# Kernel optimization log

Measured on AMD Instinct MI355X. Metric: run time of the kernel, lower is better.

Reference implementation:

```python
import jax, jax.numpy as jnp
import numpy as np

B, L, D, H = 2, 2048, 1024, 16
HD = D // H  # head_dim = 64


def setup_inputs() -> dict:
    key = jax.random.key(0)
    k1, k2, k3, k4, k5 = jax.random.split(key, 5)
    s = 1.0 / np.sqrt(D)
    return {
        "x": jax.random.normal(k1, (B, L, D), dtype=jnp.float32),
        "quantum_scores": jax.random.normal(k2, (B, L, L), dtype=jnp.float32),
        "wq": jax.random.normal(k3, (D, D), dtype=jnp.float32) * s,
        "wk": jax.random.normal(k4, (D, D), dtype=jnp.float32) * s,
        "wv": jax.random.normal(k5, (D, D), dtype=jnp.float32) * s,
        "scale": jnp.ones((H, 1, 1), dtype=jnp.float32),
    }


def reference(x, quantum_scores, wq, wk, wv, scale):
    Bq, Lq, _ = x.shape
    # nn.Linear: y = x @ W^T ; then split heads -> (B, H, L, HD)
    def split_heads(t):
        return t.reshape(Bq, Lq, H, HD).transpose(0, 2, 1, 3)

    q = split_heads(x @ wq.T)
    k = split_heads(x @ wk.T)
    v = split_heads(x @ wv.T)

    logits = jnp.einsum("bhqd,bhkd->bhqk", q, k) / np.sqrt(HD).astype(np.float32)
    logits = logits + quantum_scores[:, None, :, :]          # quantum bias, broadcast over heads
    logits = logits * scale[None, :, :, :]                   # per-head learnable scale
    attn = jax.nn.softmax(logits, axis=-1)
    out = jnp.einsum("bhqk,bhkd->bhqd", attn, v)
    return out.transpose(0, 2, 1, 3).reshape(Bq, Lq, D)
```

## Files before the change

kernel.cpp:

```cpp
#include <hip/hip_runtime.h>

#define Bq 2
#define Lq 2048
#define Dq 1024
#define Hq 16
#define HDq 64

typedef _Float16 f16;
typedef _Float16 f16x8 __attribute__((ext_vector_type(8)));
typedef _Float16 f16x4 __attribute__((ext_vector_type(4)));
typedef __fp16 hf16x2 __attribute__((ext_vector_type(2)));
typedef float f32x4 __attribute__((ext_vector_type(4)));
typedef float f32x16 __attribute__((ext_vector_type(16)));

__device__ __forceinline__ void gload_lds16(const void* g, void* l) {
    __builtin_amdgcn_global_load_lds(
        (const __attribute__((address_space(1))) unsigned int*)g,
        (__attribute__((address_space(3))) unsigned int*)l, 16, 0, 0);
}

__device__ __forceinline__ void swap32(int& a, int& b) {
    asm volatile("v_permlane32_swap_b32 %0, %1" : "+v"(a), "+v"(b));
}

__device__ __forceinline__ int pk2(float a, float b) {
    hf16x2 v = __builtin_amdgcn_cvt_pkrtz(a, b);
    return __builtin_bit_cast(int, v);
}

__global__ __launch_bounds__(256) void convert_kernel(
    const float* __restrict__ x,
    const float* __restrict__ wq, const float* __restrict__ wk, const float* __restrict__ wv,
    f16* __restrict__ x_h, f16* __restrict__ wq_h, f16* __restrict__ wk_h, f16* __restrict__ wv_h)
{
    const int NX = Bq*Lq*Dq;
    const int NW = Dq*Dq;
    const int total4 = (NX + 3*NW) / 4;
    for (int i = blockIdx.x*blockDim.x + threadIdx.x; i < total4;
         i += gridDim.x*blockDim.x) {
        int e = i * 4;
        const float* src; f16* dst; int off;
        if (e < NX) { src = x; dst = x_h; off = e; }
        else {
            int t = e - NX; int w = t >> 20; off = t & (NW-1);
            src = (w==0) ? wq : (w==1) ? wk : wv;
            dst = (w==0) ? wq_h : (w==1) ? wk_h : wv_h;
        }
        float4 v = *reinterpret_cast<const float4*>(src + off);
        f16x4 hv; hv.x=(f16)v.x; hv.y=(f16)v.y; hv.z=(f16)v.z; hv.w=(f16)v.w;
        *reinterpret_cast<f16x4*>(dst + off) = hv;
    }
}

#define GBM 128
#define GBN 128
#define GBK 32

__global__ __launch_bounds__(256) void qkv_mfma_kernel(
    const f16* __restrict__ x_h,
    const f16* __restrict__ wq_h, const f16* __restrict__ wk_h, const f16* __restrict__ wv_h,
    f16* __restrict__ q_h, f16* __restrict__ k_h, f16* __restrict__ vT_h)
{
    __shared__ __align__(16) f16 As[GBM*GBK];
    __shared__ __align__(16) f16 Bs[GBN*GBK];

    const int tid  = threadIdx.x;
    const int lane = tid & 63;
    const int wave = tid >> 6;
    const int wr = wave >> 1, wc = wave & 1;
    const int l15 = lane & 15, l4 = lane >> 4;
    const int n0 = blockIdx.x * GBN;
    const int m0 = blockIdx.y * GBM;
    const int z  = blockIdx.z;
    const f16* W = (z==0) ? wq_h : (z==1) ? wk_h : wv_h;

    const int sslot = tid & 3;

    f32x4 acc[4][4];
    #pragma unroll
    for (int i=0;i<4;++i)
        #pragma unroll
        for (int j=0;j<4;++j) acc[i][j] = f32x4{0.f,0.f,0.f,0.f};

    for (int kt = 0; kt < Dq; kt += GBK) {
        __syncthreads();
        #pragma unroll
        for (int j = 0; j < 2; ++j) {
            int slotIdx = tid + j*256;
            int row = slotIdx >> 2;
            gload_lds16(x_h + (size_t)(m0+row)*Dq + kt + sslot*8,
                        (char*)As + slotIdx*16);
            gload_lds16(W   + (size_t)(n0+row)*Dq + kt + sslot*8,
                        (char*)Bs + slotIdx*16);
        }
        __syncthreads();

        f16x8 a[4], b[4];
        #pragma unroll
        for (int m=0;m<4;++m) {
            int row = wr*64 + m*16 + l15;
            a[m] = *reinterpret_cast<const f16x8*>((const char*)As + row*64 + l4*16);
        }
        #pragma unroll
        for (int n=0;n<4;++n) {
            int row = wc*64 + n*16 + l15;
            b[n] = *reinterpret_cast<const f16x8*>((const char*)Bs + row*64 + l4*16);
        }
        #pragma unroll
        for (int m=0;m<4;++m)
            #pragma unroll
            for (int n=0;n<4;++n)
                acc[m][n] = __builtin_amdgcn_mfma_f32_16x16x32_f16(a[m], b[n], acc[m][n], 0,0,0);
    }

    #pragma unroll
    for (int m=0;m<4;++m) {
        #pragma unroll
        for (int r=0;r<4;++r) {
            int grow = m0 + wr*64 + m*16 + l4*4 + r;
            int b_   = grow >> 11;
            int lrow = grow & (Lq-1);
            #pragma unroll
            for (int n=0;n<4;++n) {
                int gcol = n0 + wc*64 + n*16 + l15;
                int h = gcol >> 6, d = gcol & 63;
                int bh = b_*Hq + h;
                f16 val = (f16)acc[m][n][r];
                if (z==0)      q_h[((size_t)bh*Lq + lrow)*HDq + d] = val;
                else if (z==1) k_h[((size_t)bh*Lq + lrow)*HDq + d] = val;
                else           vT_h[((size_t)bh*HDq + d)*Lq + lrow] = val;
            }
        }
    }
}

__global__ __launch_bounds__(256) void qm_pre_kernel(
    const float* __restrict__ quantum, float* __restrict__ qm_pre)
{
    __shared__ float qs[32][65];
    const int tid = threadIdx.x;
    const int qt = blockIdx.x, t = blockIdx.y, b = blockIdx.z;
    const float* base = quantum + ((size_t)b*Lq + qt*32)*Lq + t*64;
    #pragma unroll
    for (int i=0;i<2;++i) {
        int idx = tid + i*256;
        int r = idx >> 4, c = (idx & 15)*4;
        float4 v = *reinterpret_cast<const float4*>(base + (size_t)r*Lq + c);
        qs[r][c+0]=v.x*8.f; qs[r][c+1]=v.y*8.f; qs[r][c+2]=v.z*8.f; qs[r][c+3]=v.w*8.f;
    }
    __syncthreads();
    float* outb = qm_pre + (((size_t)b*32 + t)*64 + qt)*2048;
    #pragma unroll
    for (int i=0;i<2;++i) {
        int g = tid + i*256;
        int kt = g >> 8;
        int j  = (g >> 6) & 3;
        int lane = g & 63;
        int l31 = lane & 31, hi = lane >> 5;
        int col = kt*32 + 8*j + 4*hi;
        float4 v = { qs[l31][col], qs[l31][col+1], qs[l31][col+2], qs[l31][col+3] };
        *reinterpret_cast<float4*>(outb + ((size_t)kt*4 + j)*256 + lane*4) = v;
    }
}

__global__ __launch_bounds__(256, 2) void attn4_kernel(
    const f16* __restrict__ q_h, const f16* __restrict__ k_h, const f16* __restrict__ vT_h,
    const float* __restrict__ qm_pre, const float* __restrict__ scale,
    float* __restrict__ out)
{
    __shared__ __align__(16) char lds[49152];

    const int tid  = threadIdx.x;
    const int lane = tid & 63;
    const int wave = tid >> 6;
    const int l31  = lane & 31;
    const int hi   = lane >> 5;
    const int bh = blockIdx.x;
    const int qb = blockIdx.y;
    const int b_ = bh >> 4, h = bh & 15;
    const int qW = qb*128 + wave*32;
    const int qt = qb*4 + wave;
    const float c1 = 0.125f * scale[h] * 1.44269504f;
    const bool pos = (c1 >= 0.f);

    const f16* kbase = k_h  + (size_t)bh*Lq*HDq;
    const f16* vbase = vT_h + (size_t)bh*HDq*Lq;

    f16x8 qf[4];
    {
        const f16* qb_ = q_h + ((size_t)bh*Lq + qW + l31)*HDq + hi*8;
        #pragma unroll
        for (int ds=0; ds<4; ++ds)
            qf[ds] = *reinterpret_cast<const f16x8*>(qb_ + ds*16);
    }

    f32x16 o0, o1;
    #pragma unroll
    for (int r=0;r<16;++r) { o0[r]=0.f; o1[r]=0.f; }
    float m_run = pos ? -1e30f : 1e30f;
    float s_run = 0.f;

    auto STAGE = [&](int t, int buf) {
        const int k0 = t*64;
        char* LK = lds + buf*16384;
        char* LV = LK + 8192;
        #pragma unroll
        for (int i=0;i<2;++i) {
            int g = tid + i*256;
            int row = g >> 3, slot = g & 7;
            int ss = slot ^ (row & 7);
            gload_lds16(kbase + (size_t)(k0+row)*HDq + ss*8, LK + g*16);
            gload_lds16(vbase + (size_t)row*Lq + k0 + ss*8,  LV + g*16);
        }
    };

    auto QMLOAD = [&](int t, f32x4 (&qm)[2][4]) {
        const char* qmb = (const char*)qm_pre
            + ((((size_t)b_*32 + t)*64 + qt)*2048)*4 + lane*16;
        #pragma unroll
        for (int kt=0;kt<2;++kt)
            #pragma unroll
            for (int j=0;j<4;++j)
                qm[kt][j] = *reinterpret_cast<const f32x4*>(qmb + kt*4096 + j*1024);
    };

    auto COMPUTE = [&](int t, int buf, f32x4 (&qmc)[2][4], f32x4 (&qmn)[2][4]) {
        const char* LK = lds + buf*16384;
        const char* LV = LK + 8192;
        int tn = (t+1 < 32) ? t+1 : 31;
        QMLOAD(tn, qmn);

        f32x16 st[2];
        #pragma unroll
        for (int kt=0;kt<2;++kt)
            #pragma unroll
            for (int j=0;j<4;++j)
                #pragma unroll
                for (int c=0;c<4;++c) st[kt][4*j+c] = qmc[kt][j][c];
        __builtin_amdgcn_s_setprio(1);
        #pragma unroll
        for (int kt=0;kt<2;++kt) {
            #pragma unroll
            for (int ds=0;ds<4;++ds) {
                f16x8 ka = *reinterpret_cast<const f16x8*>(
                    LK + ((kt*32+l31)<<7) + (((ds*2+hi)^(l31&7))<<4));
                st[kt] = __builtin_amdgcn_mfma_f32_32x32x16_f16(ka, qf[ds], st[kt], 0,0,0);
            }
        }
        __builtin_amdgcn_s_setprio(0);

        float text;
        {
            float w_[16];
            if (pos) {
                #pragma unroll
                for (int r=0;r<16;++r) w_[r] = fmaxf(st[0][r], st[1][r]);
                #pragma unroll
                for (int w=8; w>0; w>>=1)
                    #pragma unroll
                    for (int r=0;r<w;++r) w_[r] = fmaxf(w_[r], w_[r+w]);
                text = fmaxf(w_[0], __shfl_xor(w_[0], 32));
            } else {
                #pragma unroll
                for (int r=0;r<16;++r) w_[r] = fminf(st[0][r], st[1][r]);
                #pragma unroll
                for (int w=8; w>0; w>>=1)
                    #pragma unroll
                    for (int r=0;r<w;++r) w_[r] = fminf(w_[r], w_[r+w]);
                text = fminf(w_[0], __shfl_xor(w_[0], 32));
            }
        }

        float u = c1*(text - m_run);
        if (!__all(u <= 8.f)) {
            float m_new = pos ? fmaxf(m_run, text) : fminf(m_run, text);
            float corr = __builtin_amdgcn_exp2f(c1*(m_run - m_new));
            m_run = m_new;
            s_run *= corr;
            #pragma unroll
            for (int r=0;r<16;++r) { o0[r] *= corr; o1[r] *= corr; }
        }

        float mb = c1 * m_run;
        float p[32];
        #pragma unroll
        for (int r=0;r<16;++r) {
            p[r]    = __builtin_amdgcn_exp2f(__builtin_fmaf(st[0][r], c1, -mb));
            p[16+r] = __builtin_amdgcn_exp2f(__builtin_fmaf(st[1][r], c1, -mb));
        }
        float sm[16];
        #pragma unroll
        for (int r=0;r<16;++r) sm[r] = p[r] + p[r+16];
        #pragma unroll
        for (int w=8; w>0; w>>=1)
            #pragma unroll
            for (int r=0;r<w;++r) sm[r] += sm[r+w];
        s_run += sm[0];

        f16x8 pb[4];
        #pragma unroll
        for (int ks=0; ks<4; ++ks) {
            int w0 = pk2(p[8*ks+0], p[8*ks+1]);
            int w1 = pk2(p[8*ks+2], p[8*ks+3]);
            int w2 = pk2(p[8*ks+4], p[8*ks+5]);
            int w3 = pk2(p[8*ks+6], p[8*ks+7]);
            swap32(w0, w2);
            swap32(w1, w3);
            union { int w[4]; f16x8 v; } u2;
            u2.w[0]=w0; u2.w[1]=w1; u2.w[2]=w2; u2.w[3]=w3;
            pb[ks] = u2.v;
        }

        __builtin_amdgcn_s_setprio(1);
        #pragma unroll
        for (int ks=0; ks<4; ++ks) {
            f16x8 va0 = *reinterpret_cast<const f16x8*>(
                LV + (l31<<7)        + (((ks*2+hi)^(l31&7))<<4));
            f16x8 va1 = *reinterpret_cast<const f16x8*>(
                LV + ((32+l31)<<7)   + (((ks*2+hi)^(l31&7))<<4));
            o0 = __builtin_amdgcn_mfma_f32_32x32x16_f16(va0, pb[ks], o0, 0,0,0);
            o1 = __builtin_amdgcn_mfma_f32_32x32x16_f16(va1, pb[ks], o1, 0,0,0);
        }
        __builtin_amdgcn_s_setprio(0);
    };

    f32x4 qmE[2][4], qmO[2][4];

    QMLOAD(0, qmE);
    STAGE(0, 0);
    STAGE(1, 1);

    #define VMW(n) asm volatile("s_waitcnt vmcnt(" #n ")" ::: "memory")

    VMW(4);  __builtin_amdgcn_s_barrier();
    STAGE(2, 2);  COMPUTE(0, 0, qmE, qmO);
    VMW(12); __builtin_amdgcn_s_barrier();
    STAGE(3, 0);  COMPUTE(1, 1, qmO, qmE);
    for (int t = 2; t < 30; t += 2) {
        VMW(20); __builtin_amdgcn_s_barrier();
        STAGE(t+2, (t+2)%3); COMPUTE(t, t%3, qmE, qmO);
        VMW(20); __builtin_amdgcn_s_barrier();
        STAGE(t+3, (t+3)%3); COMPUTE(t+1, (t+1)%3, qmO, qmE);
    }
    VMW(20); __builtin_amdgcn_s_barrier();
    COMPUTE(30, 0, qmE, qmO);
    VMW(16); __builtin_amdgcn_s_barrier();
    COMPUTE(31, 1, qmO, qmE);

    #undef VMW

    float s_tot = s_run + __shfl_xor(s_run, 32);
    float inv = 1.0f / s_tot;
    float* ob = out + ((size_t)b_*Lq + qW + l31)*Dq + h*HDq;
    #pragma unroll
    for (int r=0;r<16;++r) {
        int drow = (r&3) + 8*(r>>2) + 4*hi;
        ob[drow]      = o0[r]*inv;
        ob[32 + drow] = o1[r]*inv;
    }
}

extern "C" void kernel_launch(void* const* d_in, const int* in_sizes, int n_in,
                              void* d_out, int out_size, void* d_ws, size_t ws_size,
                              hipStream_t stream) {
    const float* x       = (const float*)d_in[0];
    const float* quantum = (const float*)d_in[1];
    const float* wq      = (const float*)d_in[2];
    const float* wk      = (const float*)d_in[3];
    const float* wv      = (const float*)d_in[4];
    const float* scale   = (const float*)d_in[5];
    float* out = (float*)d_out;

    f16* ws     = (f16*)d_ws;
    f16* x_h    = ws;
    f16* wq_h   = ws + 4194304;
    f16* wk_h   = ws + 5242880;
    f16* wv_h   = ws + 6291456;
    f16* q_h    = ws + 7340032;
    f16* k_h    = ws + 11534336;
    f16* vT_h   = ws + 15728640;
    float* qm32 = (float*)(ws + 19922944);

    convert_kernel<<<1024, 256, 0, stream>>>(x, wq, wk, wv, x_h, wq_h, wk_h, wv_h);

    dim3 gq(64, 32, 2);
    qm_pre_kernel<<<gq, 256, 0, stream>>>(quantum, qm32);

    dim3 g1(Dq/GBN, (Bq*Lq)/GBM, 3);
    qkv_mfma_kernel<<<g1, 256, 0, stream>>>(x_h, wq_h, wk_h, wv_h, q_h, k_h, vT_h);

    dim3 g2(Bq*Hq, Lq/128);
    attn4_kernel<<<g2, 256, 0, stream>>>(q_h, k_h, vT_h, qm32, scale, out);
}
```

Before: 134.8 us.

## Split attention over key dimension into two chunks with log-sum-exp combine kernel

```diff
diff --git a/kernel.cpp b/kernel.cpp
--- a/kernel.cpp
+++ b/kernel.cpp
@@ -166,7 +166,7 @@
 __global__ __launch_bounds__(256, 2) void attn4_kernel(
     const f16* __restrict__ q_h, const f16* __restrict__ k_h, const f16* __restrict__ vT_h,
     const float* __restrict__ qm_pre, const float* __restrict__ scale,
-    float* __restrict__ out)
+    f16* __restrict__ oP, float* __restrict__ tP)
 {
     __shared__ __align__(16) char lds[49152];
 
@@ -177,6 +177,8 @@
     const int hi   = lane >> 5;
     const int bh = blockIdx.x;
     const int qb = blockIdx.y;
+    const int z  = blockIdx.z;
+    const int z16 = z*16;
     const int b_ = bh >> 4, h = bh & 15;
     const int qW = qb*128 + wave*32;
     const int qt = qb*4 + wave;
@@ -201,7 +203,7 @@
     float s_run = 0.f;
 
     auto STAGE = [&](int t, int buf) {
-        const int k0 = t*64;
+        const int k0 = (z16 + t)*64;
         char* LK = lds + buf*16384;
         char* LV = LK + 8192;
         #pragma unroll
@@ -216,7 +218,7 @@
 
     auto QMLOAD = [&](int t, f32x4 (&qm)[2][4]) {
         const char* qmb = (const char*)qm_pre
-            + ((((size_t)b_*32 + t)*64 + qt)*2048)*4 + lane*16;
+            + ((((size_t)b_*32 + z16 + t)*64 + qt)*2048)*4 + lane*16;
         #pragma unroll
         for (int kt=0;kt<2;++kt)
             #pragma unroll
@@ -227,7 +229,7 @@
     auto COMPUTE = [&](int t, int buf, f32x4 (&qmc)[2][4], f32x4 (&qmn)[2][4]) {
         const char* LK = lds + buf*16384;
         const char* LV = LK + 8192;
-        int tn = (t+1 < 32) ? t+1 : 31;
+        int tn = (t+1 < 16) ? t+1 : 15;
         QMLOAD(tn, qmn);
 
         f32x16 st[2];
@@ -336,27 +338,70 @@
     STAGE(2, 2);  COMPUTE(0, 0, qmE, qmO);
     VMW(12); __builtin_amdgcn_s_barrier();
     STAGE(3, 0);  COMPUTE(1, 1, qmO, qmE);
-    for (int t = 2; t < 30; t += 2) {
+    for (int t = 2; t < 14; t += 2) {
         VMW(20); __builtin_amdgcn_s_barrier();
         STAGE(t+2, (t+2)%3); COMPUTE(t, t%3, qmE, qmO);
         VMW(20); __builtin_amdgcn_s_barrier();
         STAGE(t+3, (t+3)%3); COMPUTE(t+1, (t+1)%3, qmO, qmE);
     }
     VMW(20); __builtin_amdgcn_s_barrier();
-    COMPUTE(30, 0, qmE, qmO);
+    COMPUTE(14, 2, qmE, qmO);
     VMW(16); __builtin_amdgcn_s_barrier();
-    COMPUTE(31, 1, qmO, qmE);
+    COMPUTE(15, 0, qmO, qmE);
 
     #undef VMW
 
     float s_tot = s_run + __shfl_xor(s_run, 32);
     float inv = 1.0f / s_tot;
-    float* ob = out + ((size_t)b_*Lq + qW + l31)*Dq + h*HDq;
+    f16* obp = oP + ((size_t)(z*32 + bh)*Lq + qW + l31)*64;
     #pragma unroll
     for (int r=0;r<16;++r) {
         int drow = (r&3) + 8*(r>>2) + 4*hi;
-        ob[drow]      = o0[r]*inv;
-        ob[32 + drow] = o1[r]*inv;
+        obp[drow]      = (f16)(o0[r]*inv);
+        obp[32 + drow] = (f16)(o1[r]*inv);
+    }
+    if (hi == 0)
+        tP[(size_t)(z*32 + bh)*Lq + qW + l31] =
+            c1*m_run + __builtin_amdgcn_logf(s_tot);
+}
+
+__global__ __launch_bounds__(256) void combine_kernel(
+    const f16* __restrict__ oP, const float* __restrict__ tP,
+    float* __restrict__ out)
+{
+    const int tid = threadIdx.x;
+    const int bh = blockIdx.x, rt = blockIdx.y;
+    const int b_ = bh >> 4, h = bh & 15;
+    const int row = rt*128 + (tid >> 1);
+    const int dh = (tid & 1)*32;
+    const size_t r0 = (size_t)bh*Lq + row;
+    const size_t zr = (size_t)32*Lq;
+
+    float t0 = tP[r0], t1 = tP[zr + r0];
+    float T = fmaxf(t0, t1);
+    float w0 = __builtin_amdgcn_exp2f(t0 - T);
+    float w1 = __builtin_amdgcn_exp2f(t1 - T);
+    float inv = 1.0f/(w0 + w1);
+    w0 *= inv; w1 *= inv;
+
+    const f16* p0 = oP + r0*64 + dh;
+    const f16* p1 = oP + zr*64 + r0*64 + dh;
+    float* op = out + ((size_t)b_*Lq + row)*Dq + h*HDq + dh;
+    #pragma unroll
+    for (int j=0;j<4;++j) {
+        f16x8 a = *reinterpret_cast<const f16x8*>(p0 + j*8);
+        f16x8 b = *reinterpret_cast<const f16x8*>(p1 + j*8);
+        float4 v0, v1;
+        v0.x = (float)a[0]*w0 + (float)b[0]*w1;
+        v0.y = (float)a[1]*w0 + (float)b[1]*w1;
+        v0.z = (float)a[2]*w0 + (float)b[2]*w1;
+        v0.w = (float)a[3]*w0 + (float)b[3]*w1;
+        v1.x = (float)a[4]*w0 + (float)b[4]*w1;
+        v1.y = (float)a[5]*w0 + (float)b[5]*w1;
+        v1.z = (float)a[6]*w0 + (float)b[6]*w1;
+        v1.w = (float)a[7]*w0 + (float)b[7]*w1;
+        *reinterpret_cast<float4*>(op + j*8)     = v0;
+        *reinterpret_cast<float4*>(op + j*8 + 4) = v1;
     }
 }
 
@@ -380,6 +425,8 @@
     f16* k_h    = ws + 11534336;
     f16* vT_h   = ws + 15728640;
     float* qm32 = (float*)(ws + 19922944);
+    f16* oP     = ws + 36700160;
+    float* tP   = (float*)(ws + 45088768);
 
     convert_kernel<<<1024, 256, 0, stream>>>(x, wq, wk, wv, x_h, wq_h, wk_h, wv_h);
 
@@ -389,6 +436,9 @@
     dim3 g1(Dq/GBN, (Bq*Lq)/GBM, 3);
     qkv_mfma_kernel<<<g1, 256, 0, stream>>>(x_h, wq_h, wk_h, wv_h, q_h, k_h, vT_h);
 
-    dim3 g2(Bq*Hq, Lq/128);
-    attn4_kernel<<<g2, 256, 0, stream>>>(q_h, k_h, vT_h, qm32, scale, out);
-}
+    dim3 g2(Bq*Hq, Lq/128, 2);
+    attn4_kernel<<<g2, 256, 0, stream>>>(q_h, k_h, vT_h, qm32, scale, oP, tP);
+
+    dim3 g3(Bq*Hq, Lq/128);
+    combine_kernel<<<g3, 256, 0, stream>>>(oP, tP, out);
+}
```

After: 145.3 us. 1.08x slower.
